# Kernel tuning notes

Hardware: AMD Instinct MI355X
Metric: run time of the kernel (lower is better)

## Reference

```python
import jax, jax.numpy as jnp
import numpy as np

MARGIN = 0.1


def setup_inputs() -> dict:
    key = jax.random.key(0)
    k1, k2 = jax.random.split(key)
    scores = jax.random.normal(k1, (32, 2048), dtype=jnp.float32)
    labels = jax.random.randint(k2, (32, 2048), 0, 2, dtype=jnp.int32)
    return {"scores": scores, "labels": labels}


def reference(scores, labels):
    # scores: [B, N] float, labels: [B, N] in {0, 1}
    pos = labels == 1  # [B, N]
    neg = labels == 0  # [B, N]
    # pairwise hinge: relu(margin - pos_score_i + neg_score_j), masked to (pos, neg) pairs
    hinge = jnp.maximum(MARGIN - scores[:, :, None] + scores[:, None, :], 0.0)  # [B, N, N]
    pair_mask = pos[:, :, None] & neg[:, None, :]  # [B, N, N]
    row_sum = jnp.sum(jnp.where(pair_mask, hinge, 0.0), axis=(1, 2))  # [B]
    n_pairs = pos.sum(axis=1).astype(scores.dtype) * neg.sum(axis=1).astype(scores.dtype)  # [B]
    valid = n_pairs > 0  # rows with both pos and neg (others skipped in torch loop)
    row_loss = row_sum / jnp.maximum(n_pairs, 1.0)  # per-row pairwise mean
    n_valid = valid.sum().astype(scores.dtype)
    total = jnp.sum(jnp.where(valid, row_loss, 0.0)) / jnp.maximum(n_valid, 1.0)
    # if no valid rows, torch returns 0.0
    return jnp.where(n_valid > 0, total, jnp.asarray(0.0, scores.dtype))
```

## Files before the change

kernel.cpp:

```cpp
#include <hip/hip_runtime.h>


#define MARGIN   0.1f
#define BROWS    32
#define NCOLS    2048
#define THREADS  256
#define NWAVES   (THREADS / 64)
#define J_SPLIT  16
#define JCHUNK   (NCOLS / J_SPLIT)
#define NPART    J_SPLIT
#define KMAX     (NCOLS / THREADS)
#define NBLOCKS  (J_SPLIT * BROWS)

#define WS_NPOS  (BROWS * NPART)
#define WS_FLAG  (WS_NPOS + BROWS)
#define FLAG_TAG(i) (0x51ED0000u ^ (unsigned)(i))

template<int KC>
__device__ __forceinline__ void main_loop(const float* __restrict__ tneg,
                                          const float* __restrict__ c,
                                          float* __restrict__ acc)
{
    const float4* t4 = (const float4*)tneg;
    #pragma unroll
    for (int j8 = 0; j8 < JCHUNK / 8; ++j8) {
        const float4 v0 = t4[2 * j8];
        const float4 v1 = t4[2 * j8 + 1];
        #pragma unroll
        for (int k = 0; k < KC; ++k) {
            const float ck = c[k];
            acc[0] += fmaxf(ck + v0.x, 0.f);
            acc[1] += fmaxf(ck + v0.y, 0.f);
            acc[2] += fmaxf(ck + v0.z, 0.f);
            acc[3] += fmaxf(ck + v0.w, 0.f);
            acc[4] += fmaxf(ck + v1.x, 0.f);
            acc[5] += fmaxf(ck + v1.y, 0.f);
            acc[6] += fmaxf(ck + v1.z, 0.f);
            acc[7] += fmaxf(ck + v1.w, 0.f);
        }
    }
}

__global__ __launch_bounds__(THREADS) void rank_fused_kernel(
    const float* __restrict__ scores, const int* __restrict__ labels,
    float* __restrict__ ws, float* __restrict__ out)
{
    const int jb  = blockIdx.x;
    const int b   = blockIdx.y;
    const int bid = b * J_SPLIT + jb;

    __shared__ float tneg[JCHUNK];
    __shared__ float clist[NCOLS];
    __shared__ int   wcnt[NWAVES];
    __shared__ float wsum[NWAVES];

    const float* srow = scores + (size_t)b * NCOLS;
    const int*   lrow = labels + (size_t)b * NCOLS;
    const int tid  = threadIdx.x;
    const int lane = tid & 63;
    const int wave = tid >> 6;

    if (tid < JCHUNK) {
        const int gj = jb * JCHUNK + tid;
        const float s = srow[gj];
        tneg[tid] = (lrow[gj] == 0) ? s : -1e30f;
    }

    const float4 s0 = ((const float4*)srow)[tid * 2];
    const float4 s1 = ((const float4*)srow)[tid * 2 + 1];
    const int4   l0 = ((const int4*)lrow)[tid * 2];
    const int4   l1 = ((const int4*)lrow)[tid * 2 + 1];
    const float v[8]  = {s0.x, s0.y, s0.z, s0.w, s1.x, s1.y, s1.z, s1.w};
    const int   lb[8] = {l0.x, l0.y, l0.z, l0.w, l1.x, l1.y, l1.z, l1.w};

    int mycnt = 0;
    #pragma unroll
    for (int k = 0; k < 8; ++k) mycnt += (lb[k] == 1);

    int scan = mycnt;
    #pragma unroll
    for (int off = 1; off < 64; off <<= 1) {
        const int n = __shfl_up(scan, off, 64);
        if (lane >= off) scan += n;
    }
    if (lane == 63) wcnt[wave] = scan;
    __syncthreads();

    int wbase = 0, P = 0;
    #pragma unroll
    for (int w = 0; w < NWAVES; ++w) {
        P += wcnt[w];
        if (w < wave) wbase += wcnt[w];
    }
    int pos = wbase + (scan - mycnt);
    #pragma unroll
    for (int k = 0; k < 8; ++k)
        if (lb[k] == 1) clist[pos++] = MARGIN - v[k];
    __syncthreads();

    float c[KMAX];
    #pragma unroll
    for (int k = 0; k < KMAX; ++k) {
        const int r = k * THREADS + tid;
        c[k] = (r < P) ? clist[r] : -1e30f;
    }
    const int kcap = (P + THREADS - 1) / THREADS;

    float acc[8] = {0.f, 0.f, 0.f, 0.f, 0.f, 0.f, 0.f, 0.f};
    switch (kcap) {
        case 1: main_loop<1>(tneg, c, acc); break;
        case 2: main_loop<2>(tneg, c, acc); break;
        case 3: main_loop<3>(tneg, c, acc); break;
        case 4: main_loop<4>(tneg, c, acc); break;
        case 5: main_loop<5>(tneg, c, acc); break;
        case 6: main_loop<6>(tneg, c, acc); break;
        case 7: main_loop<7>(tneg, c, acc); break;
        case 8: main_loop<8>(tneg, c, acc); break;
        default: break;
    }
    float a = ((acc[0] + acc[1]) + (acc[2] + acc[3]))
            + ((acc[4] + acc[5]) + (acc[6] + acc[7]));

    #pragma unroll
    for (int off = 32; off >= 1; off >>= 1)
        a += __shfl_down(a, off, 64);
    if (lane == 0) wsum[wave] = a;
    __syncthreads();

    unsigned int* flags = (unsigned int*)ws + WS_FLAG;
    int*          npos  = (int*)ws + WS_NPOS;

    if (tid == 0) {
        float tot = 0.f;
        #pragma unroll
        for (int w = 0; w < NWAVES; ++w) tot += wsum[w];
        __hip_atomic_store(&ws[bid], tot,
                           __ATOMIC_RELAXED, __HIP_MEMORY_SCOPE_AGENT);
        if (jb == 0)
            __hip_atomic_store(&npos[b], P,
                               __ATOMIC_RELAXED, __HIP_MEMORY_SCOPE_AGENT);
        __hip_atomic_store(&flags[bid], FLAG_TAG(bid),
                           __ATOMIC_RELEASE, __HIP_MEMORY_SCOPE_AGENT);
    }

    if (bid == 0) {
        while (__hip_atomic_load(&flags[tid], __ATOMIC_ACQUIRE,
                                 __HIP_MEMORY_SCOPE_AGENT) != FLAG_TAG(tid))
            __builtin_amdgcn_s_sleep(1);
        while (__hip_atomic_load(&flags[tid + THREADS], __ATOMIC_ACQUIRE,
                                 __HIP_MEMORY_SCOPE_AGENT) != FLAG_TAG(tid + THREADS))
            __builtin_amdgcn_s_sleep(1);
        __syncthreads();

        if (tid < 64) {
            float loss = 0.f, valid = 0.f;
            if (tid < BROWS) {
                float s = 0.f;
                #pragma unroll
                for (int p = 0; p < NPART; ++p)
                    s += __hip_atomic_load(&ws[tid * NPART + p],
                                           __ATOMIC_RELAXED,
                                           __HIP_MEMORY_SCOPE_AGENT);
                const int np = __hip_atomic_load(&npos[tid],
                                                 __ATOMIC_RELAXED,
                                                 __HIP_MEMORY_SCOPE_AGENT);
                const int nn = NCOLS - np;
                const float pairs = (float)np * (float)nn;
                if (pairs > 0.f) { valid = 1.f; loss = s / pairs; }
            }
            #pragma unroll
            for (int off = 32; off >= 1; off >>= 1) {
                loss  += __shfl_down(loss,  off, 64);
                valid += __shfl_down(valid, off, 64);
            }
            if (tid == 0) out[0] = (valid > 0.f) ? (loss / valid) : 0.f;
        }
    }
}

extern "C" void kernel_launch(void* const* d_in, const int* in_sizes, int n_in,
                              void* d_out, int out_size, void* d_ws, size_t ws_size,
                              hipStream_t stream)
{
    const float* scores = (const float*)d_in[0];
    const int*   labels = (const int*)d_in[1];
    float* out = (float*)d_out;
    float* ws  = (float*)d_ws;

    dim3 grid(J_SPLIT, BROWS);
    rank_fused_kernel<<<grid, THREADS, 0, stream>>>(scores, labels, ws, out);
}
```

Baseline: 15.91 us.

## Compact negative columns per chunk and use ballot-based prefix scans

Each block now compacts the negative-label columns of its chunk into shared memory with ballot/mbcnt and loops only over ceil(negcnt/8) groups instead of all columns. This skips about half the hinge work per block, since roughly half the labels are positive. The shuffle-based inclusive scan for positive counts is replaced with bit-sliced ballots plus mbcnt. In exchange the inner j loop is no longer fully unrolled because its trip count is now runtime, which may reduce ILP.

```diff
diff --git a/kernel.cpp b/kernel.cpp
--- a/kernel.cpp
+++ b/kernel.cpp
@@ -8,6 +8,7 @@
 #define NWAVES   (THREADS / 64)
 #define J_SPLIT  16
 #define JCHUNK   (NCOLS / J_SPLIT)
+#define JPAD     (JCHUNK + 8)
 #define NPART    J_SPLIT
 #define KMAX     (NCOLS / THREADS)
 #define NBLOCKS  (J_SPLIT * BROWS)
@@ -16,14 +17,19 @@
 #define WS_FLAG  (WS_NPOS + BROWS)
 #define FLAG_TAG(i) (0x51ED0000u ^ (unsigned)(i))
 
+__device__ __forceinline__ int mbcnt64(unsigned long long m) {
+    return (int)__builtin_amdgcn_mbcnt_hi(
+        (unsigned)(m >> 32), __builtin_amdgcn_mbcnt_lo((unsigned)m, 0u));
+}
+
 template<int KC>
 __device__ __forceinline__ void main_loop(const float* __restrict__ tneg,
+                                          int nj8,
                                           const float* __restrict__ c,
                                           float* __restrict__ acc)
 {
     const float4* t4 = (const float4*)tneg;
-    #pragma unroll
-    for (int j8 = 0; j8 < JCHUNK / 8; ++j8) {
+    for (int j8 = 0; j8 < nj8; ++j8) {
         const float4 v0 = t4[2 * j8];
         const float4 v1 = t4[2 * j8 + 1];
         #pragma unroll
@@ -49,8 +55,9 @@
     const int b   = blockIdx.y;
     const int bid = b * J_SPLIT + jb;
 
-    __shared__ float tneg[JCHUNK];
+    __shared__ float tneg[JPAD];
     __shared__ float clist[NCOLS];
+    __shared__ int   jw[2];
     __shared__ int   wcnt[NWAVES];
     __shared__ float wsum[NWAVES];
 
@@ -60,10 +67,14 @@
     const int lane = tid & 63;
     const int wave = tid >> 6;
 
+    float jscore = 0.f; bool isneg = false; int jpre = 0;
     if (tid < JCHUNK) {
         const int gj = jb * JCHUNK + tid;
-        const float s = srow[gj];
-        tneg[tid] = (lrow[gj] == 0) ? s : -1e30f;
+        jscore = srow[gj];
+        isneg  = (lrow[gj] == 0);
+        const unsigned long long jm = __ballot(isneg);
+        jpre = mbcnt64(jm);
+        if (lane == 0) jw[wave] = (int)__popcll(jm);
     }
 
     const float4 s0 = ((const float4*)srow)[tid * 2];
@@ -77,14 +88,24 @@
     #pragma unroll
     for (int k = 0; k < 8; ++k) mycnt += (lb[k] == 1);
 
-    int scan = mycnt;
-    #pragma unroll
-    for (int off = 1; off < 64; off <<= 1) {
-        const int n = __shfl_up(scan, off, 64);
-        if (lane >= off) scan += n;
-    }
-    if (lane == 63) wcnt[wave] = scan;
+    const unsigned long long m0 = __ballot(mycnt & 1);
+    const unsigned long long m1 = __ballot(mycnt & 2);
+    const unsigned long long m2 = __ballot(mycnt & 4);
+    const unsigned long long m3 = __ballot(mycnt & 8);
+    const int ipre = mbcnt64(m0) + (mbcnt64(m1) << 1)
+                   + (mbcnt64(m2) << 2) + (mbcnt64(m3) << 3);
+    if (lane == 0)
+        wcnt[wave] = (int)__popcll(m0) + ((int)__popcll(m1) << 1)
+                   + ((int)__popcll(m2) << 2) + ((int)__popcll(m3) << 3);
     __syncthreads();
+
+    const int negcnt = jw[0] + jw[1];
+    const int nj8    = (negcnt + 7) >> 3;
+    const int npj    = nj8 << 3;
+    if (tid < JCHUNK && isneg)
+        tneg[(tid < 64 ? 0 : jw[0]) + jpre] = jscore;
+    if (tid >= negcnt && tid < npj)
+        tneg[tid] = -1e30f;
 
     int wbase = 0, P = 0;
     #pragma unroll
@@ -92,7 +113,7 @@
         P += wcnt[w];
         if (w < wave) wbase += wcnt[w];
     }
-    int pos = wbase + (scan - mycnt);
+    int pos = wbase + ipre;
     #pragma unroll
     for (int k = 0; k < 8; ++k)
         if (lb[k] == 1) clist[pos++] = MARGIN - v[k];
@@ -108,14 +129,14 @@
 
     float acc[8] = {0.f, 0.f, 0.f, 0.f, 0.f, 0.f, 0.f, 0.f};
     switch (kcap) {
-        case 1: main_loop<1>(tneg, c, acc); break;
-        case 2: main_loop<2>(tneg, c, acc); break;
-        case 3: main_loop<3>(tneg, c, acc); break;
-        case 4: main_loop<4>(tneg, c, acc); break;
-        case 5: main_loop<5>(tneg, c, acc); break;
-        case 6: main_loop<6>(tneg, c, acc); break;
-        case 7: main_loop<7>(tneg, c, acc); break;
-        case 8: main_loop<8>(tneg, c, acc); break;
+        case 1: main_loop<1>(tneg, nj8, c, acc); break;
+        case 2: main_loop<2>(tneg, nj8, c, acc); break;
+        case 3: main_loop<3>(tneg, nj8, c, acc); break;
+        case 4: main_loop<4>(tneg, nj8, c, acc); break;
+        case 5: main_loop<5>(tneg, nj8, c, acc); break;
+        case 6: main_loop<6>(tneg, nj8, c, acc); break;
+        case 7: main_loop<7>(tneg, nj8, c, acc); break;
+        case 8: main_loop<8>(tneg, nj8, c, acc); break;
         default: break;
     }
     float a = ((acc[0] + acc[1]) + (acc[2] + acc[3]))
```

Result: faster. 14.95 us (-6.0%).
